# Performance work log

Hardware: AMD Instinct MI355X
Metric: run time of the kernel (lower is better)

Reference implementation:

```python
import jax, jax.numpy as jnp
import numpy as np

T, N, D = 64, 40, 4
H, R, K = 256, 64, 2
E = N * (N - 1)


def _xavier(key, shape):
    std = (2.0 / (shape[0] + shape[1])) ** 0.5
    return (std * jax.random.normal(key, shape)).astype(jnp.float32)


def setup_inputs() -> dict:
    ks = iter(jax.random.split(jax.random.key(0), 40))
    send, recv = np.where(np.ones((N, N)) - np.eye(N))  # fully-connected directed graph, E = N*(N-1)
    p = {}
    p['inputs'] = jax.random.normal(next(ks), (1, T, N, D), dtype=jnp.float32)
    p['node_masks'] = jnp.ones((1, T, N), dtype=jnp.float32)
    p['send_edges'] = jnp.asarray(send, dtype=jnp.int32)
    p['recv_edges'] = jnp.asarray(recv, dtype=jnp.int32)
    for name, nin in (('mlp1', D), ('mlp2', 2 * H), ('mlp3', H), ('mlp4', 3 * H)):
        p[name + '_W1'] = _xavier(next(ks), (H, nin))
        p[name + '_b1'] = jnp.full((H,), 0.1, jnp.float32)
        p[name + '_W2'] = _xavier(next(ks), (H, H))
        p[name + '_b2'] = jnp.full((H,), 0.1, jnp.float32)
    s = float(1.0 / np.sqrt(R))
    for nm in ('fwd', 'rev'):
        p[nm + '_Wih'] = jax.random.uniform(next(ks), (4 * R, H), jnp.float32, -s, s)
        p[nm + '_Whh'] = jax.random.uniform(next(ks), (4 * R, R), jnp.float32, -s, s)
        p[nm + '_bih'] = jnp.zeros((4 * R,), jnp.float32)
        p[nm + '_bhh'] = jnp.zeros((4 * R,), jnp.float32)
    p['enc_W'] = _xavier(next(ks), (K, 2 * R))
    p['enc_b'] = jnp.full((K,), 0.1, jnp.float32)
    p['prior_W'] = _xavier(next(ks), (K, R))
    p['prior_b'] = jnp.full((K,), 0.1, jnp.float32)
    return p


def _mlp(x, W1, b1, W2, b2):
    # RefNRIMLP in eval mode with no_bn=True: elu(fc2(elu(fc1(x))))
    return jax.nn.elu(jax.nn.elu(x @ W1.T + b1) @ W2.T + b2)


def _lstm(xs, Wih, Whh, bih, bhh):
    # xs: [T, E, H] -> hidden states [T, E, R]; PyTorch LSTM gate order i, f, g, o
    def step(carry, xt):
        h, c = carry
        g = xt @ Wih.T + bih + h @ Whh.T + bhh
        i, f, gg, o = jnp.split(g, 4, axis=-1)
        c = jax.nn.sigmoid(f) * c + jax.nn.sigmoid(i) * jnp.tanh(gg)
        h = jax.nn.sigmoid(o) * jnp.tanh(c)
        return (h, c), h
    Rh = Whh.shape[1]
    init = (jnp.zeros((xs.shape[1], Rh), xs.dtype), jnp.zeros((xs.shape[1], Rh), xs.dtype))
    _, hs = jax.lax.scan(step, init, xs)
    return hs


def _encode(inputs, send, recv,
            m1W1, m1b1, m1W2, m1b2, m2W1, m2b1, m2W2, m2b2,
            m3W1, m3b1, m3W2, m3b2, m4W1, m4b1, m4W2, m4b2,
            fWih, fWhh, fbih, fbhh, rWih, rWhh, rbih, rbhh,
            encW, encb, priW, prib):
    x = inputs[0]                                                  # [T, N, D]
    h = _mlp(x, m1W1, m1b1, m1W2, m1b2)                            # [T, N, H]
    e = jnp.concatenate([h[:, send], h[:, recv]], axis=-1)         # node2edge gather [T, E, 2H]
    e = _mlp(e, m2W1, m2b1, m2W2, m2b2)                            # [T, E, H]
    skip = e
    n = jnp.zeros((x.shape[0], x.shape[1], e.shape[-1]), e.dtype)
    n = n.at[:, recv].add(e)                                       # edge2node scatter-add (index_add_)
    n = _mlp(n, m3W1, m3b1, m3W2, m3b2)                            # [T, N, H]
    e = jnp.concatenate([n[:, send], n[:, recv], skip], axis=-1)   # [T, E, 3H]
    e = _mlp(e, m4W1, m4b1, m4W2, m4b2)                            # per-edge features over time [T, E, H]
    fwd_h = _lstm(e, fWih, fWhh, fbih, fbhh)                       # [T, E, R]
    rev_h = _lstm(e[::-1], rWih, rWhh, rbih, rbhh)[::-1]           # [T, E, R]
    prior = fwd_h @ priW.T + prib                                  # [T, E, K]
    enc = jnp.concatenate([fwd_h, rev_h], axis=-1) @ encW.T + encb # [T, E, K]
    return jnp.concatenate([prior, enc], axis=-1)                  # [T, E, 2K]


def reference(inputs, node_masks, send_edges, recv_edges,
              mlp1_W1, mlp1_b1, mlp1_W2, mlp1_b2,
              mlp2_W1, mlp2_b1, mlp2_W2, mlp2_b2,
              mlp3_W1, mlp3_b1, mlp3_W2, mlp3_b2,
              mlp4_W1, mlp4_b1, mlp4_W2, mlp4_b2,
              fwd_Wih, fwd_Whh, fwd_bih, fwd_bhh,
              rev_Wih, rev_Whh, rev_bih, rev_bhh,
              enc_W, enc_b, prior_W, prior_b):
    del node_masks  # all nodes present -> static fully-connected graph each step
    return _encode(inputs, send_edges, recv_edges,
                   mlp1_W1, mlp1_b1, mlp1_W2, mlp1_b2,
                   mlp2_W1, mlp2_b1, mlp2_W2, mlp2_b2,
                   mlp3_W1, mlp3_b1, mlp3_W2, mlp3_b2,
                   mlp4_W1, mlp4_b1, mlp4_W2, mlp4_b2,
                   fwd_Wih, fwd_Whh, fwd_bih, fwd_bhh,
                   rev_Wih, rev_Whh, rev_bih, rev_bhh,
                   enc_W, enc_b, prior_W, prior_b)
```

## Files before the change

### kernel.cpp

```cpp
#include <hip/hip_runtime.h>
#include <math.h>

#define T_ 64
#define N_ 40
#define D_ 4
#define H_ 256
#define R_ 64
#define E_ 1560
#define TE_ (T_*E_)
#define TN_ (T_*N_)

typedef unsigned short us;
typedef short short8 __attribute__((ext_vector_type(8)));
typedef float f32x4 __attribute__((ext_vector_type(4)));

__device__ __forceinline__ float elu_f(float x){ return x > 0.f ? x : (__expf(x) - 1.f); }
__device__ __forceinline__ float sig_f(float x){ return 1.f/(1.f+__expf(-x)); }
__device__ __forceinline__ float tanh_f(float x){ return 2.f/(1.f+__expf(-2.f*x)) - 1.f; }
__device__ __forceinline__ float dot4(float4 a, float4 b){ return a.x*b.x + a.y*b.y + a.z*b.z + a.w*b.w; }

__device__ __forceinline__ float bf2f(us u){ return __uint_as_float(((unsigned int)u) << 16); }
__device__ __forceinline__ us f2bf(float f){
    unsigned int u = __float_as_uint(f);
    u += 0x7FFFu + ((u >> 16) & 1u);
    return (us)(u >> 16);
}
__device__ __forceinline__ float4 ld4f(const float* p){ return *(const float4*)p; }
__device__ __forceinline__ float4 ld4f(const us* p){
    ushort4 v = *(const ushort4*)p;
    return make_float4(bf2f(v.x), bf2f(v.y), bf2f(v.z), bf2f(v.w));
}
__device__ __forceinline__ void st4f(float* p, float4 v){ *(float4*)p = v; }
__device__ __forceinline__ void st4f(us* p, float4 v){
    ushort4 o; o.x = f2bf(v.x); o.y = f2bf(v.y); o.z = f2bf(v.z); o.w = f2bf(v.w);
    *(ushort4*)p = o;
}

__device__ __forceinline__ void gld16(void* lds, const void* g){
    __builtin_amdgcn_global_load_lds((const __attribute__((address_space(1))) unsigned int*)g,
                                     (__attribute__((address_space(3))) unsigned int*)lds,
                                     16, 0, 0);
}

__device__ __forceinline__ void wsplit1(const float* W, us* hi, us* lo, int i){
    const float w = W[i];
    const us h = f2bf(w);
    hi[i] = h;
    lo[i] = f2bf(w - bf2f(h));
}

__global__ __launch_bounds__(256)
void wsplit_all(const float* __restrict__ s0, us* h0, us* l0,
                const float* __restrict__ s1, us* h1, us* l1,
                const float* __restrict__ s2, us* h2, us* l2,
                const float* __restrict__ s3, us* h3, us* l3,
                const float* __restrict__ s4, us* h4, us* l4,
                const float* __restrict__ s5, us* h5, us* l5,
                const float* __restrict__ s6, us* h6, us* l6,
                const float* __restrict__ s7, us* h7, us* l7)
{
    int i = blockIdx.x * 256 + threadIdx.x;
    if (i < 131072) { wsplit1(s0, h0, l0, i); return; } i -= 131072;
    if (i <  65536) { wsplit1(s1, h1, l1, i); return; } i -=  65536;
    if (i < 196608) { wsplit1(s2, h2, l2, i); return; } i -= 196608;
    if (i <  65536) { wsplit1(s3, h3, l3, i); return; } i -=  65536;
    if (i <  65536) { wsplit1(s4, h4, l4, i); return; } i -=  65536;
    if (i <  65536) { wsplit1(s5, h5, l5, i); return; } i -=  65536;
    if (i <  16384) { wsplit1(s6, h6, l6, i); return; } i -=  16384;
    wsplit1(s7, h7, l7, i);
}

__global__ __launch_bounds__(256)
void mlp1_kernel(const float* __restrict__ x,
                 const float* __restrict__ W1, const float* __restrict__ b1,
                 const float* __restrict__ W2, const float* __restrict__ b2,
                 us* __restrict__ hout)
{
    __shared__ float xs[8][4];
    __shared__ float h1[8][256];
    const int tid = threadIdx.x;
    const int r0  = blockIdx.x * 8;

    if (tid < 32) xs[tid >> 2][tid & 3] = x[r0 * 4 + tid];
    __syncthreads();

    const float4 w1 = *(const float4*)&W1[tid * 4];
    const float bb1 = b1[tid];
    #pragma unroll
    for (int row = 0; row < 8; ++row) {
        float v = bb1 + xs[row][0]*w1.x + xs[row][1]*w1.y + xs[row][2]*w1.z + xs[row][3]*w1.w;
        h1[row][tid] = elu_f(v);
    }
    __syncthreads();

    float acc[8];
    const float bb2 = b2[tid];
    #pragma unroll
    for (int row = 0; row < 8; ++row) acc[row] = bb2;
    const float* w2row = W2 + (size_t)tid * 256;
    for (int k4 = 0; k4 < 64; ++k4) {
        const float4 w = *(const float4*)&w2row[k4 * 4];
        #pragma unroll
        for (int row = 0; row < 8; ++row) {
            const float4 hh = *(const float4*)&h1[row][k4 * 4];
            acc[row] += dot4(hh, w);
        }
    }
    #pragma unroll
    for (int row = 0; row < 8; ++row)
        hout[(size_t)(r0 + row) * 256 + tid] = f2bf(elu_f(acc[row]));
}

template<int MODE, bool DOELU>
__global__ __launch_bounds__(256, 2)
void gemm_mfma(const us* __restrict__ A, const us* __restrict__ A2, const us* __restrict__ A3,
               const us* __restrict__ Whi, const us* __restrict__ Wlo,
               const float* __restrict__ bias1, const float* __restrict__ bias2,
               const int* __restrict__ send, const int* __restrict__ recv,
               us* __restrict__ C, int Kdim,
               const us* __restrict__ Whi2, const us* __restrict__ Wlo2,
               const float* __restrict__ bias1b, const float* __restrict__ bias2b,
               us* __restrict__ C2)
{
    __shared__ char smem[65536];

    const int tid  = threadIdx.x;
    const int lane = tid & 63;
    const int w    = tid >> 6;
    const int ml   = lane & 15;
    const int q    = lane >> 4;
    const int bx   = blockIdx.x;
    int by         = blockIdx.y;
    const int eh   = w >> 1;
    const int fh   = w & 1;

    if (MODE == 0 && C2 != nullptr && by >= 2) {
        Whi = Whi2; Wlo = Wlo2; bias1 = bias1b; bias2 = bias2b; C = C2; by -= 2;
    }

    const int lr   = lane >> 2;
    const int cofs = (((lane & 3) ^ ((lane >> 3) & 3)) * 8);

    const us *pA0[4], *pA1[4], *pA2v[4];
    #pragma unroll
    for (int i = 0; i < 4; ++i) {
        const int gr = bx * 256 + i * 64 + w * 16 + lr;
        if (MODE == 0) {
            pA0[i] = A + (size_t)gr * Kdim;
            pA1[i] = nullptr; pA2v[i] = nullptr;
        } else {
            const int t = gr / E_, e = gr - t * E_;
            pA0[i] = A  + ((size_t)(t * N_ + send[e])) * H_;
            pA1[i] = A2 + ((size_t)(t * N_ + recv[e])) * H_;
            pA2v[i] = (MODE == 2) ? (A3 + (size_t)gr * H_) : nullptr;
        }
    }
    const us *pWh[2], *pWl[2];
    #pragma unroll
    for (int j = 0; j < 2; ++j) {
        const int wr = by * 128 + j * 64 + w * 16 + lr;
        pWh[j] = Whi + (size_t)wr * Kdim;
        pWl[j] = Wlo + (size_t)wr * Kdim;
    }

    f32x4 acc[4][8];
    #pragma unroll
    for (int i = 0; i < 4; ++i)
        #pragma unroll
        for (int j = 0; j < 8; ++j)
            acc[i][j] = (f32x4){0.f, 0.f, 0.f, 0.f};

    auto stage = [&](int k0, char* base) {
        #pragma unroll
        for (int i = 0; i < 4; ++i) {
            const us* sa;
            if (MODE == 0)      sa = pA0[i] + k0;
            else if (MODE == 1) sa = (k0 < 256) ? pA0[i] + k0 : pA1[i] + (k0 - 256);
            else                sa = (k0 < 256) ? pA0[i] + k0
                                   : (k0 < 512) ? pA1[i] + (k0 - 256)
                                                : pA2v[i] + (k0 - 512);
            gld16(base + (i * 4 + w) * 1024, sa + cofs);
        }
        #pragma unroll
        for (int j = 0; j < 2; ++j) {
            gld16(base + 16384 + (j * 4 + w) * 1024, pWh[j] + k0 + cofs);
            gld16(base + 24576 + (j * 4 + w) * 1024, pWl[j] + k0 + cofs);
        }
    };

    const int qs16 = (q ^ ((ml >> 1) & 3)) * 16;

    stage(0, smem);
    const int nk = Kdim >> 5;
    for (int k = 0; k < nk; ++k) {
        char* cur = smem + (k & 1) * 32768;
        char* nxt = smem + ((k + 1) & 1) * 32768;
        __builtin_amdgcn_s_barrier();
        if (k + 1 < nk) {
            stage((k + 1) * 32, nxt);
            __builtin_amdgcn_s_waitcnt(0x3F78);
        } else {
            __builtin_amdgcn_s_waitcnt(0x3F70);
        }
        __builtin_amdgcn_s_barrier();

        short8 wh[4], wl[4], ef[8];
        #pragma unroll
        for (int mt = 0; mt < 4; ++mt) {
            const int blkOf = (fh * 4 + mt) * 1024 + ml * 64 + qs16;
            wh[mt] = *(const short8*)(cur + 16384 + blkOf);
            wl[mt] = *(const short8*)(cur + 24576 + blkOf);
        }
        #pragma unroll
        for (int nt = 0; nt < 8; ++nt) {
            const int blkOf = (eh * 8 + nt) * 1024 + ml * 64 + qs16;
            ef[nt] = *(const short8*)(cur + blkOf);
        }
        #pragma unroll
        for (int nt = 0; nt < 8; ++nt)
            #pragma unroll
            for (int mt = 0; mt < 4; ++mt) {
                acc[mt][nt] = __builtin_amdgcn_mfma_f32_16x16x32_bf16(wh[mt], ef[nt], acc[mt][nt], 0, 0, 0);
                acc[mt][nt] = __builtin_amdgcn_mfma_f32_16x16x32_bf16(wl[mt], ef[nt], acc[mt][nt], 0, 0, 0);
            }
    }

    #pragma unroll
    for (int mt = 0; mt < 4; ++mt) {
        const int colb = by * 128 + fh * 64 + mt * 16 + q * 4;
        float4 bb = *(const float4*)(bias1 + colb);
        if (bias2) {
            const float4 b2 = *(const float4*)(bias2 + colb);
            bb.x += b2.x; bb.y += b2.y; bb.z += b2.z; bb.w += b2.w;
        }
        #pragma unroll
        for (int nt = 0; nt < 8; ++nt) {
            const int row = bx * 256 + eh * 128 + nt * 16 + ml;
            float4 v;
            v.x = acc[mt][nt][0] + bb.x; v.y = acc[mt][nt][1] + bb.y;
            v.z = acc[mt][nt][2] + bb.z; v.w = acc[mt][nt][3] + bb.w;
            if (DOELU) { v.x = elu_f(v.x); v.y = elu_f(v.y); v.z = elu_f(v.z); v.w = elu_f(v.w); }
            ushort4 o; o.x = f2bf(v.x); o.y = f2bf(v.y); o.z = f2bf(v.z); o.w = f2bf(v.w);
            *(ushort4*)(C + (size_t)row * 256 + colb) = o;
        }
    }
}

template<bool DOELU, typename TA, typename TC>
__global__ __launch_bounds__(256)
void gemm_nt(const TA* __restrict__ A, const float* __restrict__ W,
             const float* __restrict__ bias1,
             TC* __restrict__ C, int M, int Kdim)
{
    __shared__ float As[16][64];
    __shared__ float Ws[16][64];

    const int tid = threadIdx.x;
    const int am  = tid >> 2;
    const int ak  = (tid & 3) * 4;
    const int gm  = blockIdx.x * 64 + am;

    const TA* aptr0 = A + (size_t)gm * Kdim;
    const float* wptr = W + (size_t)(blockIdx.y * 64 + am) * Kdim;

    const int tx = tid & 15, ty = tid >> 4;
    float acc[4][4] = {};

    for (int k0 = 0; k0 < Kdim; k0 += 16) {
        const float4 a4 = ld4f(aptr0 + k0 + ak);
        const float4 w4 = *(const float4*)(wptr + k0 + (tid & 3) * 4);

        __syncthreads();
        As[ak+0][am] = a4.x; As[ak+1][am] = a4.y; As[ak+2][am] = a4.z; As[ak+3][am] = a4.w;
        const int wk = (tid & 3) * 4;
        Ws[wk+0][am] = w4.x; Ws[wk+1][am] = w4.y; Ws[wk+2][am] = w4.z; Ws[wk+3][am] = w4.w;
        __syncthreads();

        #pragma unroll
        for (int kq = 0; kq < 16; ++kq) {
            const float4 av = *(const float4*)&As[kq][ty * 4];
            const float4 wv = *(const float4*)&Ws[kq][tx * 4];
            const float a_[4] = {av.x, av.y, av.z, av.w};
            const float w_[4] = {wv.x, wv.y, wv.z, wv.w};
            #pragma unroll
            for (int i = 0; i < 4; ++i)
                #pragma unroll
                for (int j = 0; j < 4; ++j)
                    acc[i][j] += a_[i] * w_[j];
        }
    }

    const int gn = blockIdx.y * 64 + tx * 4;
    const float4 bb = *(const float4*)&bias1[gn];
    #pragma unroll
    for (int i = 0; i < 4; ++i) {
        const int row = blockIdx.x * 64 + ty * 4 + i;
        float4 o;
        o.x = acc[i][0] + bb.x; o.y = acc[i][1] + bb.y;
        o.z = acc[i][2] + bb.z; o.w = acc[i][3] + bb.w;
        if (DOELU) { o.x = elu_f(o.x); o.y = elu_f(o.y); o.z = elu_f(o.z); o.w = elu_f(o.w); }
        st4f(C + (size_t)row * 256 + gn, o);
    }
}

__global__ __launch_bounds__(256)
void aggregate_kernel(const us* __restrict__ eSkip, const int* __restrict__ recv,
                      float* __restrict__ nAgg)
{
    const int t = blockIdx.x / N_;
    const int j = blockIdx.x - t * N_;
    const int c = threadIdx.x;
    const us* basep = eSkip + (size_t)t * E_ * H_ + c;
    float acc = 0.f;
    #pragma unroll
    for (int s = 0; s < N_; ++s) {
        if (s == j) continue;
        const int e = s * (N_ - 1) + (j < s ? j : j - 1);
        acc += bf2f(basep[(size_t)e * H_]);
    }
    nAgg[(size_t)blockIdx.x * H_ + c] = acc;
}

__global__ __launch_bounds__(256)
void lstm_mfma(const us* __restrict__ Gf, const us* __restrict__ Gr,
               const us* __restrict__ fWhhH, const us* __restrict__ fWhhL,
               const us* __restrict__ rWhhH, const us* __restrict__ rWhhL,
               float* __restrict__ hsF, float* __restrict__ hsR)
{
    const int NBD = (E_ + 15) / 16;
    const bool revd = (int)blockIdx.x >= NBD;
    const int blk = revd ? (int)blockIdx.x - NBD : (int)blockIdx.x;
    const int e0 = blk * 16;
    const us* G  = revd ? Gr : Gf;
    const us* WH = revd ? rWhhH : fWhhH;
    const us* WL = revd ? rWhhL : fWhhL;
    float* hs    = revd ? hsR : hsF;

    const int tid  = threadIdx.x;
    const int lane = tid & 63;
    const int w    = tid >> 6;
    const int ml   = lane & 15;
    const int q    = lane >> 4;

    __shared__ us hHi[2][16][72];
    __shared__ us hLo[2][16][72];

    short8 wfh[4][2], wfl[4][2];
    #pragma unroll
    for (int mt = 0; mt < 4; ++mt) {
        const int row = mt * 64 + w * 16 + ml;
        #pragma unroll
        for (int ks = 0; ks < 2; ++ks) {
            wfh[mt][ks] = *(const short8*)(WH + (size_t)row * 64 + ks * 32 + q * 8);
            wfl[mt][ks] = *(const short8*)(WL + (size_t)row * 64 + ks * 32 + q * 8);
        }
    }

    for (int i = tid; i < 16 * 72; i += 256) { (&hHi[0][0][0])[i] = 0; (&hLo[0][0][0])[i] = 0; }

    const int eMF = min(e0 + ml, E_ - 1);
    const bool wr = (e0 + ml) < E_;
    const int gOfs = w * 16 + q * 4;
    float4 cst = make_float4(0.f, 0.f, 0.f, 0.f);

    ushort4 gcur[4], gnxt[4];
    {
        const int tt0 = revd ? (T_ - 1) : 0;
        const us* gp = G + ((size_t)tt0 * E_ + eMF) * 256 + gOfs;
        #pragma unroll
        for (int mt = 0; mt < 4; ++mt) gcur[mt] = *(const ushort4*)(gp + mt * 64);
    }
    __syncthreads();

    for (int s = 0; s < T_; ++s) {
        const int tt = revd ? (T_ - 1 - s) : s;
        {
            const int sn = (s + 1 < T_) ? s + 1 : s;
            const int tn = revd ? (T_ - 1 - sn) : sn;
            const us* gp = G + ((size_t)tn * E_ + eMF) * 256 + gOfs;
            #pragma unroll
            for (int mt = 0; mt < 4; ++mt) gnxt[mt] = *(const ushort4*)(gp + mt * 64);
        }
        const int rb = s & 1, wb = rb ^ 1;
        short8 bh[2], bl[2];
        #pragma unroll
        for (int ks = 0; ks < 2; ++ks) {
            bh[ks] = *(const short8*)(&hHi[rb][ml][ks * 32 + q * 8]);
            bl[ks] = *(const short8*)(&hLo[rb][ml][ks * 32 + q * 8]);
        }
        f32x4 acc[4];
        #pragma unroll
        for (int mt = 0; mt < 4; ++mt) {
            acc[mt][0] = bf2f(gcur[mt].x); acc[mt][1] = bf2f(gcur[mt].y);
            acc[mt][2] = bf2f(gcur[mt].z); acc[mt][3] = bf2f(gcur[mt].w);
            #pragma unroll
            for (int ks = 0; ks < 2; ++ks) {
                acc[mt] = __builtin_amdgcn_mfma_f32_16x16x32_bf16(wfh[mt][ks], bh[ks], acc[mt], 0, 0, 0);
                acc[mt] = __builtin_amdgcn_mfma_f32_16x16x32_bf16(wfh[mt][ks], bl[ks], acc[mt], 0, 0, 0);
                acc[mt] = __builtin_amdgcn_mfma_f32_16x16x32_bf16(wfl[mt][ks], bh[ks], acc[mt], 0, 0, 0);
            }
        }
        float4 hv;
        cst.x = sig_f(acc[1][0])*cst.x + sig_f(acc[0][0])*tanh_f(acc[2][0]); hv.x = sig_f(acc[3][0])*tanh_f(cst.x);
        cst.y = sig_f(acc[1][1])*cst.y + sig_f(acc[0][1])*tanh_f(acc[2][1]); hv.y = sig_f(acc[3][1])*tanh_f(cst.y);
        cst.z = sig_f(acc[1][2])*cst.z + sig_f(acc[0][2])*tanh_f(acc[2][2]); hv.z = sig_f(acc[3][2])*tanh_f(cst.z);
        cst.w = sig_f(acc[1][3])*cst.w + sig_f(acc[0][3])*tanh_f(acc[2][3]); hv.w = sig_f(acc[3][3])*tanh_f(cst.w);
        ushort4 hh4, hl4;
        hh4.x = f2bf(hv.x); hl4.x = f2bf(hv.x - bf2f(hh4.x));
        hh4.y = f2bf(hv.y); hl4.y = f2bf(hv.y - bf2f(hh4.y));
        hh4.z = f2bf(hv.z); hl4.z = f2bf(hv.z - bf2f(hh4.z));
        hh4.w = f2bf(hv.w); hl4.w = f2bf(hv.w - bf2f(hh4.w));
        *(ushort4*)(&hHi[wb][ml][gOfs]) = hh4;
        *(ushort4*)(&hLo[wb][ml][gOfs]) = hl4;
        if (wr)
            *(float4*)(&hs[((size_t)tt * E_ + e0 + ml) * 64 + gOfs]) = hv;
        __syncthreads();
        #pragma unroll
        for (int mt = 0; mt < 4; ++mt) gcur[mt] = gnxt[mt];
    }
}

__global__ __launch_bounds__(256)
void out_kernel(const float* __restrict__ hsF, const float* __restrict__ hsR,
                const float* __restrict__ priW, const float* __restrict__ prib,
                const float* __restrict__ encW, const float* __restrict__ encb,
                float* __restrict__ out)
{
    const int idx = blockIdx.x * 256 + threadIdx.x;
    const float* f = hsF + (size_t)idx * 64;
    const float* r = hsR + (size_t)idx * 64;
    float p0 = prib[0], p1 = prib[1], q0 = encb[0], q1 = encb[1];
    #pragma unroll
    for (int k4 = 0; k4 < 16; ++k4) {
        const float4 fv = *(const float4*)(f + k4 * 4);
        const float4 rv = *(const float4*)(r + k4 * 4);
        p0 += dot4(fv, *(const float4*)(priW + k4 * 4));
        p1 += dot4(fv, *(const float4*)(priW + 64 + k4 * 4));
        q0 += dot4(fv, *(const float4*)(encW + k4 * 4))
            + dot4(rv, *(const float4*)(encW + 64 + k4 * 4));
        q1 += dot4(fv, *(const float4*)(encW + 128 + k4 * 4))
            + dot4(rv, *(const float4*)(encW + 192 + k4 * 4));
    }
    float4 o; o.x = p0; o.y = p1; o.z = q0; o.w = q1;
    *(float4*)(out + (size_t)idx * 4) = o;
}

extern "C" void kernel_launch(void* const* d_in, const int* in_sizes, int n_in,
                              void* d_out, int out_size, void* d_ws, size_t ws_size,
                              hipStream_t stream)
{
    const float* x    = (const float*)d_in[0];
    const int*   send = (const int*)d_in[2];
    const int*   recv = (const int*)d_in[3];
    const float* m1W1 = (const float*)d_in[4];  const float* m1b1 = (const float*)d_in[5];
    const float* m1W2 = (const float*)d_in[6];  const float* m1b2 = (const float*)d_in[7];
    const float* m2W1 = (const float*)d_in[8];  const float* m2b1 = (const float*)d_in[9];
    const float* m2W2 = (const float*)d_in[10]; const float* m2b2 = (const float*)d_in[11];
    const float* m3W1 = (const float*)d_in[12]; const float* m3b1 = (const float*)d_in[13];
    const float* m3W2 = (const float*)d_in[14]; const float* m3b2 = (const float*)d_in[15];
    const float* m4W1 = (const float*)d_in[16]; const float* m4b1 = (const float*)d_in[17];
    const float* m4W2 = (const float*)d_in[18]; const float* m4b2 = (const float*)d_in[19];
    const float* fWih = (const float*)d_in[20]; const float* fWhh = (const float*)d_in[21];
    const float* fbih = (const float*)d_in[22]; const float* fbhh = (const float*)d_in[23];
    const float* rWih = (const float*)d_in[24]; const float* rWhh = (const float*)d_in[25];
    const float* rbih = (const float*)d_in[26]; const float* rbhh = (const float*)d_in[27];
    const float* encW = (const float*)d_in[28]; const float* encb = (const float*)d_in[29];
    const float* priW = (const float*)d_in[30]; const float* prib = (const float*)d_in[31];

    const size_t SZN  = (size_t)TN_ * H_;
    const size_t SZE  = (size_t)TE_ * H_;
    float* n_agg = (float*)d_ws;
    float* m3t   = n_agg + SZN;
    us* h16      = (us*)(m3t + SZN);
    us* n3       = h16 + SZN;
    us* w2aH = n3  + SZN;          us* w2aL = w2aH + 256*512;
    us* w2bH = w2aL + 256*512;     us* w2bL = w2bH + 256*256;
    us* w4aH = w2bL + 256*256;     us* w4aL = w4aH + 256*768;
    us* w4bH = w4aL + 256*768;     us* w4bL = w4bH + 256*256;
    us* wfiH = w4bL + 256*256;     us* wfiL = wfiH + 256*256;
    us* wriH = wfiL + 256*256;     us* wriL = wriH + 256*256;
    us* whfH = wriL + 256*256;     us* whfL = whfH + 256*64;
    us* whrH = whfL + 256*64;      us* whrL = whrH + 256*64;
    us* bufA16 = whrL + 256*64;
    us* bufB16 = bufA16 + SZE;
    us* bufC16 = bufB16 + SZE;
    float* hsF = (float*)bufC16;
    float* hsR = hsF + (size_t)TE_ * R_;
    const size_t needed = ((size_t)(bufC16 + SZE) - (size_t)d_ws);
    if (ws_size < needed) return;

    const dim3 gMF(TE_ / 256, 2), gMF4(TE_ / 256, 4), gN(TN_ / 64, 4);
    const us* z = nullptr; const float* zf = nullptr; us* zo = nullptr;

    wsplit_all<<<2432, 256, 0, stream>>>(m2W1, w2aH, w2aL, m2W2, w2bH, w2bL,
                                         m4W1, w4aH, w4aL, m4W2, w4bH, w4bL,
                                         fWih, wfiH, wfiL, rWih, wriH, wriL,
                                         fWhh, whfH, whfL, rWhh, whrH, whrL);

    mlp1_kernel<<<TN_ / 8, 256, 0, stream>>>(x, m1W1, m1b1, m1W2, m1b2, h16);
    gemm_mfma<1, true><<<gMF, 256, 0, stream>>>(h16, h16, nullptr, w2aH, w2aL, m2b1, nullptr, send, recv, bufA16, 512, z, z, zf, zf, zo);
    gemm_mfma<0, true><<<gMF, 256, 0, stream>>>(bufA16, nullptr, nullptr, w2bH, w2bL, m2b2, nullptr, send, recv, bufB16, 256, z, z, zf, zf, zo);
    aggregate_kernel<<<TN_, 256, 0, stream>>>(bufB16, recv, n_agg);
    gemm_nt<true, float, float><<<gN, 256, 0, stream>>>(n_agg, m3W1, m3b1, m3t, TN_, 256);
    gemm_nt<true, float, us><<<gN, 256, 0, stream>>>(m3t, m3W2, m3b2, n3, TN_, 256);
    gemm_mfma<2, true><<<gMF, 256, 0, stream>>>(n3, n3, bufB16, w4aH, w4aL, m4b1, nullptr, send, recv, bufA16, 768, z, z, zf, zf, zo);
    gemm_mfma<0, true><<<gMF, 256, 0, stream>>>(bufA16, nullptr, nullptr, w4bH, w4bL, m4b2, nullptr, send, recv, bufC16, 256, z, z, zf, zf, zo);
    gemm_mfma<0, false><<<gMF4, 256, 0, stream>>>(bufC16, nullptr, nullptr, wfiH, wfiL, fbih, fbhh, send, recv, bufA16, 256,
                                                  wriH, wriL, rbih, rbhh, bufB16);
    lstm_mfma<<<2 * ((E_ + 15) / 16), 256, 0, stream>>>(bufA16, bufB16, whfH, whfL, whrH, whrL, hsF, hsR);
    out_kernel<<<TE_ / 256, 256, 0, stream>>>(hsF, hsR, priW, prib, encW, encb, (float*)d_out);
}
```

Baseline: 598.3 us.

## Factor edge-concat first layers into per-node projections gathered per edge

The first layers of mlp2 and mlp4 act on concatenated [sender, receiver(, edge)] features. Because the weight matrix splits by column block, the sender and receiver parts are now computed once per node (2560 rows) in a new node_proj kernel and then gathered per edge. This replaces a K=512 edge GEMM with a gather+ELU kernel, and turns the K=768 edge GEMM into a K=256 GEMM whose epilogue adds the gathered node projections. The cost is extra fp32 projection tables, gather traffic in the epilogue, and node projections done in plain fp32 FMA rather than split-bf16 MFMA, which changes numerics slightly.

Result: faster. 568.4 us (-5.0%).

```diff
diff --git a/kernel.cpp b/kernel.cpp
--- a/kernel.cpp
+++ b/kernel.cpp
@@ -56,18 +56,22 @@
                 const float* __restrict__ s3, us* h3, us* l3,
                 const float* __restrict__ s4, us* h4, us* l4,
                 const float* __restrict__ s5, us* h5, us* l5,
-                const float* __restrict__ s6, us* h6, us* l6,
-                const float* __restrict__ s7, us* h7, us* l7)
+                const float* __restrict__ s6, us* h6, us* l6)
 {
     int i = blockIdx.x * 256 + threadIdx.x;
-    if (i < 131072) { wsplit1(s0, h0, l0, i); return; } i -= 131072;
-    if (i <  65536) { wsplit1(s1, h1, l1, i); return; } i -=  65536;
-    if (i < 196608) { wsplit1(s2, h2, l2, i); return; } i -= 196608;
-    if (i <  65536) { wsplit1(s3, h3, l3, i); return; } i -=  65536;
-    if (i <  65536) { wsplit1(s4, h4, l4, i); return; } i -=  65536;
-    if (i <  65536) { wsplit1(s5, h5, l5, i); return; } i -=  65536;
-    if (i <  16384) { wsplit1(s6, h6, l6, i); return; } i -=  16384;
-    wsplit1(s7, h7, l7, i);
+    if (i < 65536) { wsplit1(s0, h0, l0, i); return; } i -= 65536;
+    if (i < 65536) {
+        const float w = s1[(i >> 8) * 768 + 512 + (i & 255)];
+        const us h = f2bf(w);
+        h1[i] = h;
+        l1[i] = f2bf(w - bf2f(h));
+        return;
+    } i -= 65536;
+    if (i < 65536) { wsplit1(s2, h2, l2, i); return; } i -= 65536;
+    if (i < 65536) { wsplit1(s3, h3, l3, i); return; } i -= 65536;
+    if (i < 65536) { wsplit1(s4, h4, l4, i); return; } i -= 65536;
+    if (i < 16384) { wsplit1(s5, h5, l5, i); return; } i -= 16384;
+    wsplit1(s6, h6, l6, i);
 }
 
 __global__ __launch_bounds__(256)
@@ -111,12 +115,88 @@
         hout[(size_t)(r0 + row) * 256 + tid] = f2bf(elu_f(acc[row]));
 }
 
+__global__ __launch_bounds__(256)
+void node_proj(const us* __restrict__ A, const float* __restrict__ W,
+               int wstride, float* __restrict__ P)
+{
+    __shared__ float As[16][64];
+    __shared__ float Ws[16][64];
+
+    const int tid  = threadIdx.x;
+    const int am   = tid >> 2;
+    const int gm   = blockIdx.x * 64 + am;
+    const int part = blockIdx.y >> 2;
+    const int wq   = blockIdx.y & 3;
+
+    const us* aptr = A + (size_t)gm * 256;
+    const float* wptr = W + (size_t)(wq * 64 + am) * wstride + part * 256;
+
+    const int tx = tid & 15, ty = tid >> 4;
+    float acc[4][4] = {};
+
+    for (int k0 = 0; k0 < 256; k0 += 16) {
+        const float4 a4 = ld4f(aptr + k0 + (tid & 3) * 4);
+        const float4 w4 = *(const float4*)(wptr + k0 + (tid & 3) * 4);
+
+        __syncthreads();
+        const int ak = (tid & 3) * 4;
+        As[ak+0][am] = a4.x; As[ak+1][am] = a4.y; As[ak+2][am] = a4.z; As[ak+3][am] = a4.w;
+        Ws[ak+0][am] = w4.x; Ws[ak+1][am] = w4.y; Ws[ak+2][am] = w4.z; Ws[ak+3][am] = w4.w;
+        __syncthreads();
+
+        #pragma unroll
+        for (int kq = 0; kq < 16; ++kq) {
+            const float4 av = *(const float4*)&As[kq][ty * 4];
+            const float4 wv = *(const float4*)&Ws[kq][tx * 4];
+            const float a_[4] = {av.x, av.y, av.z, av.w};
+            const float w_[4] = {wv.x, wv.y, wv.z, wv.w};
+            #pragma unroll
+            for (int i = 0; i < 4; ++i)
+                #pragma unroll
+                for (int j = 0; j < 4; ++j)
+                    acc[i][j] += a_[i] * w_[j];
+        }
+    }
+
+    const int gn = part * 256 + wq * 64 + tx * 4;
+    #pragma unroll
+    for (int i = 0; i < 4; ++i) {
+        const int row = blockIdx.x * 64 + ty * 4 + i;
+        float4 o;
+        o.x = acc[i][0]; o.y = acc[i][1]; o.z = acc[i][2]; o.w = acc[i][3];
+        *(float4*)(P + (size_t)row * 512 + gn) = o;
+    }
+}
+
+__global__ __launch_bounds__(256)
+void edge_gather_elu(const float* __restrict__ P, const float* __restrict__ b1,
+                     const int* __restrict__ send, const int* __restrict__ recv,
+                     us* __restrict__ out)
+{
+    const int tid = threadIdx.x;
+    const int r   = blockIdx.x * 4 + (tid >> 6);
+    const int c4  = (tid & 63) * 4;
+    const int t = r / E_;
+    const int e = r - t * E_;
+    const float4 a  = *(const float4*)(P + ((size_t)(t * N_ + send[e])) * 512 + c4);
+    const float4 b  = *(const float4*)(P + ((size_t)(t * N_ + recv[e])) * 512 + 256 + c4);
+    const float4 bb = *(const float4*)(b1 + c4);
+    float4 v;
+    v.x = elu_f(a.x + b.x + bb.x);
+    v.y = elu_f(a.y + b.y + bb.y);
+    v.z = elu_f(a.z + b.z + bb.z);
+    v.w = elu_f(a.w + b.w + bb.w);
+    ushort4 o; o.x = f2bf(v.x); o.y = f2bf(v.y); o.z = f2bf(v.z); o.w = f2bf(v.w);
+    *(ushort4*)(out + (size_t)r * 256 + c4) = o;
+}
+
 template<int MODE, bool DOELU>
 __global__ __launch_bounds__(256, 2)
-void gemm_mfma(const us* __restrict__ A, const us* __restrict__ A2, const us* __restrict__ A3,
+void gemm_mfma(const us* __restrict__ A,
                const us* __restrict__ Whi, const us* __restrict__ Wlo,
                const float* __restrict__ bias1, const float* __restrict__ bias2,
                const int* __restrict__ send, const int* __restrict__ recv,
+               const float* __restrict__ Ptab,
                us* __restrict__ C, int Kdim,
                const us* __restrict__ Whi2, const us* __restrict__ Wlo2,
                const float* __restrict__ bias1b, const float* __restrict__ bias2b,
@@ -141,19 +221,11 @@
     const int lr   = lane >> 2;
     const int cofs = (((lane & 3) ^ ((lane >> 3) & 3)) * 8);
 
-    const us *pA0[4], *pA1[4], *pA2v[4];
+    const us* pA0[4];
     #pragma unroll
     for (int i = 0; i < 4; ++i) {
         const int gr = bx * 256 + i * 64 + w * 16 + lr;
-        if (MODE == 0) {
-            pA0[i] = A + (size_t)gr * Kdim;
-            pA1[i] = nullptr; pA2v[i] = nullptr;
-        } else {
-            const int t = gr / E_, e = gr - t * E_;
-            pA0[i] = A  + ((size_t)(t * N_ + send[e])) * H_;
-            pA1[i] = A2 + ((size_t)(t * N_ + recv[e])) * H_;
-            pA2v[i] = (MODE == 2) ? (A3 + (size_t)gr * H_) : nullptr;
-        }
+        pA0[i] = A + (size_t)gr * Kdim;
     }
     const us *pWh[2], *pWl[2];
     #pragma unroll
@@ -172,15 +244,8 @@
 
     auto stage = [&](int k0, char* base) {
         #pragma unroll
-        for (int i = 0; i < 4; ++i) {
-            const us* sa;
-            if (MODE == 0)      sa = pA0[i] + k0;
-            else if (MODE == 1) sa = (k0 < 256) ? pA0[i] + k0 : pA1[i] + (k0 - 256);
-            else                sa = (k0 < 256) ? pA0[i] + k0
-                                   : (k0 < 512) ? pA1[i] + (k0 - 256)
-                                                : pA2v[i] + (k0 - 512);
-            gld16(base + (i * 4 + w) * 1024, sa + cofs);
-        }
+        for (int i = 0; i < 4; ++i)
+            gld16(base + (i * 4 + w) * 1024, pA0[i] + k0 + cofs);
         #pragma unroll
         for (int j = 0; j < 2; ++j) {
             gld16(base + 16384 + (j * 4 + w) * 1024, pWh[j] + k0 + cofs);
@@ -225,6 +290,18 @@
             }
     }
 
+    int srowA[8], rrowA[8];
+    if (MODE == 3) {
+        #pragma unroll
+        for (int nt = 0; nt < 8; ++nt) {
+            const int row = bx * 256 + eh * 128 + nt * 16 + ml;
+            const int t = row / E_;
+            const int e = row - t * E_;
+            srowA[nt] = t * N_ + send[e];
+            rrowA[nt] = t * N_ + recv[e];
+        }
+    }
+
     #pragma unroll
     for (int mt = 0; mt < 4; ++mt) {
         const int colb = by * 128 + fh * 64 + mt * 16 + q * 4;
@@ -239,6 +316,12 @@
             float4 v;
             v.x = acc[mt][nt][0] + bb.x; v.y = acc[mt][nt][1] + bb.y;
             v.z = acc[mt][nt][2] + bb.z; v.w = acc[mt][nt][3] + bb.w;
+            if (MODE == 3) {
+                const float4 pS = *(const float4*)(Ptab + (size_t)srowA[nt] * 512 + colb);
+                const float4 pR = *(const float4*)(Ptab + (size_t)rrowA[nt] * 512 + 256 + colb);
+                v.x += pS.x + pR.x; v.y += pS.y + pR.y;
+                v.z += pS.z + pR.z; v.w += pS.w + pR.w;
+            }
             if (DOELU) { v.x = elu_f(v.x); v.y = elu_f(v.y); v.z = elu_f(v.z); v.w = elu_f(v.w); }
             ushort4 o; o.x = f2bf(v.x); o.y = f2bf(v.y); o.z = f2bf(v.z); o.w = f2bf(v.w);
             *(ushort4*)(C + (size_t)row * 256 + colb) = o;
@@ -471,17 +554,17 @@
     const size_t SZE  = (size_t)TE_ * H_;
     float* n_agg = (float*)d_ws;
     float* m3t   = n_agg + SZN;
+    float* Ptab  = (float*)d_ws;
     us* h16      = (us*)(m3t + SZN);
     us* n3       = h16 + SZN;
-    us* w2aH = n3  + SZN;          us* w2aL = w2aH + 256*512;
-    us* w2bH = w2aL + 256*512;     us* w2bL = w2bH + 256*256;
-    us* w4aH = w2bL + 256*256;     us* w4aL = w4aH + 256*768;
-    us* w4bH = w4aL + 256*768;     us* w4bL = w4bH + 256*256;
-    us* wfiH = w4bL + 256*256;     us* wfiL = wfiH + 256*256;
-    us* wriH = wfiL + 256*256;     us* wriL = wriH + 256*256;
-    us* whfH = wriL + 256*256;     us* whfL = whfH + 256*64;
-    us* whrH = whfL + 256*64;      us* whrL = whrH + 256*64;
-    us* bufA16 = whrL + 256*64;
+    us* w2bH = n3  + SZN;          us* w2bL = w2bH + 65536;
+    us* w4aH = w2bL + 65536;       us* w4aL = w4aH + 65536;
+    us* w4bH = w4aL + 65536;       us* w4bL = w4bH + 65536;
+    us* wfiH = w4bL + 65536;       us* wfiL = wfiH + 65536;
+    us* wriH = wfiL + 65536;       us* wriL = wriH + 65536;
+    us* whfH = wriL + 65536;       us* whfL = whfH + 16384;
+    us* whrH = whfL + 16384;       us* whrL = whrH + 16384;
+    us* bufA16 = whrL + 16384;
     us* bufB16 = bufA16 + SZE;
     us* bufC16 = bufB16 + SZE;
     float* hsF = (float*)bufC16;
@@ -489,23 +572,26 @@
     const size_t needed = ((size_t)(bufC16 + SZE) - (size_t)d_ws);
     if (ws_size < needed) return;
 
-    const dim3 gMF(TE_ / 256, 2), gMF4(TE_ / 256, 4), gN(TN_ / 64, 4);
+    const dim3 gMF(TE_ / 256, 2), gMF4(TE_ / 256, 4), gN(TN_ / 64, 4), gNP(TN_ / 64, 8);
     const us* z = nullptr; const float* zf = nullptr; us* zo = nullptr;
 
-    wsplit_all<<<2432, 256, 0, stream>>>(m2W1, w2aH, w2aL, m2W2, w2bH, w2bL,
-                                         m4W1, w4aH, w4aL, m4W2, w4bH, w4bL,
+    wsplit_all<<<1408, 256, 0, stream>>>(m2W2, w2bH, w2bL,
+                                         m4W1, w4aH, w4aL,
+                                         m4W2, w4bH, w4bL,
                                          fWih, wfiH, wfiL, rWih, wriH, wriL,
                                          fWhh, whfH, whfL, rWhh, whrH, whrL);
 
     mlp1_kernel<<<TN_ / 8, 256, 0, stream>>>(x, m1W1, m1b1, m1W2, m1b2, h16);
-    gemm_mfma<1, true><<<gMF, 256, 0, stream>>>(h16, h16, nullptr, w2aH, w2aL, m2b1, nullptr, send, recv, bufA16, 512, z, z, zf, zf, zo);
-    gemm_mfma<0, true><<<gMF, 256, 0, stream>>>(bufA16, nullptr, nullptr, w2bH, w2bL, m2b2, nullptr, send, recv, bufB16, 256, z, z, zf, zf, zo);
+    node_proj<<<gNP, 256, 0, stream>>>(h16, m2W1, 512, Ptab);
+    edge_gather_elu<<<TE_ / 4, 256, 0, stream>>>(Ptab, m2b1, send, recv, bufA16);
+    gemm_mfma<0, true><<<gMF, 256, 0, stream>>>(bufA16, w2bH, w2bL, m2b2, nullptr, send, recv, zf, bufB16, 256, z, z, zf, zf, zo);
     aggregate_kernel<<<TN_, 256, 0, stream>>>(bufB16, recv, n_agg);
     gemm_nt<true, float, float><<<gN, 256, 0, stream>>>(n_agg, m3W1, m3b1, m3t, TN_, 256);
     gemm_nt<true, float, us><<<gN, 256, 0, stream>>>(m3t, m3W2, m3b2, n3, TN_, 256);
-    gemm_mfma<2, true><<<gMF, 256, 0, stream>>>(n3, n3, bufB16, w4aH, w4aL, m4b1, nullptr, send, recv, bufA16, 768, z, z, zf, zf, zo);
-    gemm_mfma<0, true><<<gMF, 256, 0, stream>>>(bufA16, nullptr, nullptr, w4bH, w4bL, m4b2, nullptr, send, recv, bufC16, 256, z, z, zf, zf, zo);
-    gemm_mfma<0, false><<<gMF4, 256, 0, stream>>>(bufC16, nullptr, nullptr, wfiH, wfiL, fbih, fbhh, send, recv, bufA16, 256,
+    node_proj<<<gNP, 256, 0, stream>>>(n3, m4W1, 768, Ptab);
+    gemm_mfma<3, true><<<gMF, 256, 0, stream>>>(bufB16, w4aH, w4aL, m4b1, nullptr, send, recv, Ptab, bufA16, 256, z, z, zf, zf, zo);
+    gemm_mfma<0, true><<<gMF, 256, 0, stream>>>(bufA16, w4bH, w4bL, m4b2, nullptr, send, recv, zf, bufC16, 256, z, z, zf, zf, zo);
+    gemm_mfma<0, false><<<gMF4, 256, 0, stream>>>(bufC16, wfiH, wfiL, fbih, fbhh, send, recv, zf, bufA16, 256,
                                                   wriH, wriL, rbih, rbhh, bufB16);
     lstm_mfma<<<2 * ((E_ + 15) / 16), 256, 0, stream>>>(bufA16, bufB16, whfH, whfL, whrH, whrL, hsF, hsR);
     out_kernel<<<TE_ / 256, 256, 0, stream>>>(hsF, hsR, priW, prib, encW, encb, (float*)d_out);
```
